# Kernel optimization log

Measured on AMD Instinct MI355X. Metric: run time of the kernel, lower is better.

The kernel has to match this reference:

```python
import jax, jax.numpy as jnp
import numpy as np

ENDING = False  # ending=False -> 'outgoing' triangle update; True -> 'incoming'
EPS = 1e-5


def _ln(x, w, b):
    m = jnp.mean(x, axis=-1, keepdims=True)
    v = jnp.mean((x - m) ** 2, axis=-1, keepdims=True)
    return (x - m) * jax.lax.rsqrt(v + EPS) * w + b


def setup_inputs() -> dict:
    key = jax.random.key(0)
    ks = jax.random.split(key, 6)
    B, N, D = 1, 384, 128
    s = 0.02
    return {
        "x": jax.random.normal(ks[0], (B, N, N, D), jnp.float32),
        "norm_in_w": jnp.ones((D,), jnp.float32),
        "norm_in_b": jnp.zeros((D,), jnp.float32),
        "w_g_in": jax.random.normal(ks[1], (2 * D, D), jnp.float32) * s,
        "w_p_in": jax.random.normal(ks[2], (2 * D, D), jnp.float32) * s,
        "w_g_out": jax.random.normal(ks[3], (D, D), jnp.float32) * s,
        "norm_out_w": jnp.ones((D,), jnp.float32),
        "norm_out_b": jnp.zeros((D,), jnp.float32),
        "w_p_out": jax.random.normal(ks[4], (D, D), jnp.float32) * s,
    }


def reference(x, norm_in_w, norm_in_b, w_g_in, w_p_in, w_g_out,
              norm_out_w, norm_out_b, w_p_out):
    D = x.shape[-1]
    xn = _ln(x, norm_in_w, norm_in_b)                       # [B,N,N,D]
    g_in = jax.nn.sigmoid(jnp.einsum('bijd,ed->bije', xn, w_g_in))  # [B,N,N,2D]
    p = jnp.einsum('bijd,ed->bije', xn, w_p_in) * g_in      # [B,N,N,2D]
    a, b = p[..., :D], p[..., D:]
    if ENDING:
        # incoming: out[i,j,d] = sum_k a[k,i,d] * b[k,j,d]
        t = jnp.einsum('bkid,bkjd->bijd', a, b)
    else:
        # outgoing: out[i,j,d] = sum_k a[i,k,d] * b[j,k,d]
        t = jnp.einsum('bikd,bjkd->bijd', a, b)
    g_out = jax.nn.sigmoid(jnp.einsum('bijd,ed->bije', xn, w_g_out))  # [B,N,N,D]
    return g_out * jnp.einsum('bijd,ed->bije', _ln(t, norm_out_w, norm_out_b), w_p_out)
```

## Files before the change

kernel.cpp:

```cpp
#include <hip/hip_runtime.h>
#include <hip/hip_bf16.h>
#include <math.h>

#define NPOS 147456
#define NSEQ 384

typedef __attribute__((ext_vector_type(4))) float f32x4;
typedef __attribute__((ext_vector_type(8))) short bf16x8;
typedef __attribute__((ext_vector_type(4))) short s16x4;

__device__ __forceinline__ unsigned short f2bf(float f){
  union { float f; unsigned u; } v; v.f = f;
  unsigned r = v.u + 0x7FFFu + ((v.u >> 16) & 1u);
  return (unsigned short)(r >> 16);
}
__device__ __forceinline__ float bf2f(unsigned short h){
  union { unsigned u; float f; } v; v.u = ((unsigned)h) << 16;
  return v.f;
}
__device__ __forceinline__ float fastsig(float x){
  return __builtin_amdgcn_rcpf(1.0f + __expf(-x));
}
__device__ __forceinline__ unsigned pk2(float lo, float hi){
  return (unsigned)f2bf(lo) | ((unsigned)f2bf(hi) << 16);
}

__global__ void wswz_all(const float* __restrict__ wgi, const float* __restrict__ wpi,
                         const float* __restrict__ wgo, const float* __restrict__ wpo,
                         unsigned short* __restrict__ wgi_s, unsigned short* __restrict__ wpi_s,
                         unsigned short* __restrict__ wgo_s, unsigned short* __restrict__ wpo_s){
  int i = blockIdx.x * 256 + threadIdx.x;
  int t = i >> 11;
  int r = i & 2047;
  const float* src; unsigned short* dst; int lt;
  if (t < 16)      { src = wgi; dst = wgi_s; lt = t;      }
  else if (t < 32) { src = wpi; dst = wpi_s; lt = t - 16; }
  else if (t < 40) { src = wgo; dst = wgo_s; lt = t - 32; }
  else             { src = wpo; dst = wpo_s; lt = t - 40; }
  int j = r & 7, lane = (r >> 3) & 63, kk = (r >> 9) & 3;
  int lrow = lane & 15, khh = lane >> 4;
  dst[lt*2048 + r] = f2bf(src[(lt*16 + lrow)*128 + kk*32 + khh*8 + j]);
}

__global__ __launch_bounds__(256, 3) void k1_ln_proj(
    const float* __restrict__ x,
    const float* __restrict__ ln_w, const float* __restrict__ ln_b,
    const unsigned short* __restrict__ wg_sw,
    const unsigned short* __restrict__ wp_sw,
    const unsigned short* __restrict__ wgo_sw,
    unsigned short* __restrict__ a_t,
    unsigned short* __restrict__ b_t,
    unsigned short* __restrict__ g_t)
{
  __shared__ unsigned short xn[128][128];
  unsigned short (*obuf)[16][136] = reinterpret_cast<unsigned short(*)[16][136]>(&xn[0][0]);

  const int tid  = threadIdx.x;
  const int posb = blockIdx.x * 128;
  const int lane = tid & 63;
  const int wid  = tid >> 6;

  const int rql = tid >> 2;
  const int q   = tid & 3;
  #pragma unroll
  for (int rr = 0; rr < 2; ++rr){
    int row = rr*64 + rql;
    const float* xr = x + (size_t)(posb + row) * 128 + q * 32;
    float v[32]; float s = 0.f, s2 = 0.f;
    #pragma unroll
    for (int j2 = 0; j2 < 8; ++j2){
      f32x4 t4 = *(const f32x4*)(xr + j2*4);
      #pragma unroll
      for (int m = 0; m < 4; ++m){ float f = t4[m]; v[j2*4+m] = f; s += f; s2 += f*f; }
    }
    s  += __shfl_xor(s, 1);  s  += __shfl_xor(s, 2);
    s2 += __shfl_xor(s2, 1); s2 += __shfl_xor(s2, 2);
    float mean = s * (1.f/128.f);
    float rstd = rsqrtf(s2 * (1.f/128.f) - mean*mean + 1e-5f);
    int sw = (row & 7) * 8;
    #pragma unroll
    for (int c = 0; c < 4; ++c){
      float n[8];
      #pragma unroll
      for (int j2 = 0; j2 < 8; ++j2){
        int k = q*32 + c*8 + j2;
        n[j2] = (v[c*8+j2] - mean) * rstd * ln_w[k] + ln_b[k];
      }
      uint4 u;
      u.x = pk2(n[0], n[1]); u.y = pk2(n[2], n[3]);
      u.z = pk2(n[4], n[5]); u.w = pk2(n[6], n[7]);
      *(uint4*)&xn[row][(q*32 + c*8) ^ sw] = u;
    }
  }
  __syncthreads();

  const int lrow = lane & 15, kh = lane >> 4;
  bf16x8 afrag[2][4];
  #pragma unroll
  for (int r = 0; r < 2; ++r){
    int row = wid*32 + r*16 + lrow;
    int sw = (row & 7) * 8;
    #pragma unroll
    for (int kk = 0; kk < 4; ++kk)
      afrag[r][kk] = *(const bf16x8*)&xn[row][(kk*32 + kh*8) ^ sw];
  }
  __syncthreads();

  const int kh4 = kh * 4;
  const int scl = wid*4 + kh;
  const int spo = lrow * 8;

#define LOADW_PAIR(G, P, et) do { \
    const unsigned short* _wg = wg_sw + (size_t)(et)*2048 + lane*8; \
    const unsigned short* _wp = wp_sw + (size_t)(et)*2048 + lane*8; \
    _Pragma("unroll") \
    for (int kk = 0; kk < 4; ++kk){ \
      G[kk] = *(const bf16x8*)(_wg + kk*512); \
      P[kk] = *(const bf16x8*)(_wp + kk*512); \
    } } while(0)

#define COMPUTE_PAIR(G, P, et) do { \
    f32x4 accg0 = {0.f,0.f,0.f,0.f}, accg1 = {0.f,0.f,0.f,0.f}; \
    f32x4 accp0 = {0.f,0.f,0.f,0.f}, accp1 = {0.f,0.f,0.f,0.f}; \
    _Pragma("unroll") \
    for (int kk = 0; kk < 4; ++kk){ \
      accg0 = __builtin_amdgcn_mfma_f32_16x16x32_bf16(afrag[0][kk], G[kk], accg0, 0, 0, 0); \
      accg1 = __builtin_amdgcn_mfma_f32_16x16x32_bf16(afrag[1][kk], G[kk], accg1, 0, 0, 0); \
      accp0 = __builtin_amdgcn_mfma_f32_16x16x32_bf16(afrag[0][kk], P[kk], accp0, 0, 0, 0); \
      accp1 = __builtin_amdgcn_mfma_f32_16x16x32_bf16(afrag[1][kk], P[kk], accp1, 0, 0, 0); \
    } \
    { uint2 u0, u1; \
      u0.x = pk2(fastsig(accg0[0])*accp0[0], fastsig(accg0[1])*accp0[1]); \
      u0.y = pk2(fastsig(accg0[2])*accp0[2], fastsig(accg0[3])*accp0[3]); \
      u1.x = pk2(fastsig(accg1[0])*accp1[0], fastsig(accg1[1])*accp1[1]); \
      u1.y = pk2(fastsig(accg1[2])*accp1[2], fastsig(accg1[3])*accp1[3]); \
      *(uint2*)&obuf[(et)&1][lrow][wid*32 + kh4]      = u0; \
      *(uint2*)&obuf[(et)&1][lrow][wid*32 + 16 + kh4] = u1; } \
    __syncthreads(); \
    { bf16x8 vv = *(const bf16x8*)&obuf[(et)&1][scl][spo]; \
      int colg = (et)*16 + scl; \
      unsigned short* dst = ((et) < 8) ? (a_t + (size_t)colg * NPOS) \
                                       : (b_t + (size_t)(colg - 128) * NPOS); \
      *(bf16x8*)(dst + posb + spo) = vv; } \
  } while(0)

  {
    bf16x8 gA[4], pA[4], gB[4], pB[4];
    LOADW_PAIR(gA, pA, 0);
    #pragma unroll
    for (int e2 = 0; e2 < 8; ++e2){
      LOADW_PAIR(gB, pB, e2*2 + 1);
      COMPUTE_PAIR(gA, pA, e2*2);
      if (e2 < 7) LOADW_PAIR(gA, pA, e2*2 + 2);
      COMPUTE_PAIR(gB, pB, e2*2 + 1);
    }
  }

#define LOADW_G(Q, et) do { \
    const unsigned short* _wq = wgo_sw + (size_t)(et)*2048 + lane*8; \
    _Pragma("unroll") \
    for (int kk = 0; kk < 4; ++kk) Q[kk] = *(const bf16x8*)(_wq + kk*512); \
  } while(0)

#define COMPUTE_G(Q, et) do { \
    f32x4 a0 = {0.f,0.f,0.f,0.f}, a1 = {0.f,0.f,0.f,0.f}; \
    _Pragma("unroll") \
    for (int kk = 0; kk < 4; ++kk){ \
      a0 = __builtin_amdgcn_mfma_f32_16x16x32_bf16(afrag[0][kk], Q[kk], a0, 0, 0, 0); \
      a1 = __builtin_amdgcn_mfma_f32_16x16x32_bf16(afrag[1][kk], Q[kk], a1, 0, 0, 0); \
    } \
    { uint2 u0, u1; \
      u0.x = pk2(fastsig(a0[0]), fastsig(a0[1])); \
      u0.y = pk2(fastsig(a0[2]), fastsig(a0[3])); \
      u1.x = pk2(fastsig(a1[0]), fastsig(a1[1])); \
      u1.y = pk2(fastsig(a1[2]), fastsig(a1[3])); \
      *(uint2*)&obuf[(et)&1][lrow][wid*32 + kh4]      = u0; \
      *(uint2*)&obuf[(et)&1][lrow][wid*32 + 16 + kh4] = u1; } \
    __syncthreads(); \
    { bf16x8 vv = *(const bf16x8*)&obuf[(et)&1][scl][spo]; \
      *(bf16x8*)(g_t + (size_t)((et)*16 + scl) * NPOS + posb + spo) = vv; } \
  } while(0)

  {
    bf16x8 qA[4], qB[4];
    LOADW_G(qA, 0);
    #pragma unroll
    for (int e2 = 0; e2 < 4; ++e2){
      LOADW_G(qB, e2*2 + 1);
      COMPUTE_G(qA, e2*2);
      if (e2 < 3) LOADW_G(qA, e2*2 + 2);
      COMPUTE_G(qB, e2*2 + 1);
    }
  }
#undef LOADW_PAIR
#undef COMPUTE_PAIR
#undef LOADW_G
#undef COMPUTE_G
}

#define K2S 72
__global__ __launch_bounds__(256) void k2_tri(
    const unsigned short* __restrict__ a_t,
    const unsigned short* __restrict__ b_t,
    unsigned short* __restrict__ t_t)
{
  __shared__ unsigned short smem[128 * K2S * 2];
  unsigned short (*As)[K2S] = (unsigned short (*)[K2S])smem;
  unsigned short (*Bs)[K2S] = (unsigned short (*)[K2S])(smem + 128 * K2S);

  const int bid  = blockIdx.x;
  const int gg   = bid >> 3;
  const int d    = (bid & 7) + 8 * (gg / 9);
  const int tile = gg % 9;
  const int i0 = (tile / 3) * 128;
  const int j0 = (tile % 3) * 128;
  const unsigned short* Ab = a_t + (size_t)d * NPOS;
  const unsigned short* Bb = b_t + (size_t)d * NPOS;

  const int tid = threadIdx.x;
  const int wid = tid >> 6, lane = tid & 63;
  const int wr = wid >> 1, wc = wid & 1;
  const int lrow = lane & 15, kh = (lane >> 4) * 8;

  f32x4 acc[4][4];
  #pragma unroll
  for (int r = 0; r < 4; ++r)
    #pragma unroll
    for (int c = 0; c < 4; ++c)
      acc[r][c] = (f32x4){0.f,0.f,0.f,0.f};

  const int sr = tid >> 1, sc = (tid & 1) * 32;

  for (int k0 = 0; k0 < NSEQ; k0 += 64){
    bf16x8 va[4], vb[4];
    #pragma unroll
    for (int j = 0; j < 4; ++j){
      va[j] = *(const bf16x8*)(Ab + (size_t)(i0 + sr) * NSEQ + k0 + sc + j*8);
      vb[j] = *(const bf16x8*)(Bb + (size_t)(j0 + sr) * NSEQ + k0 + sc + j*8);
    }
    __syncthreads();
    #pragma unroll
    for (int j = 0; j < 4; ++j){
      *(bf16x8*)&As[sr][sc + j*8] = va[j];
      *(bf16x8*)&Bs[sr][sc + j*8] = vb[j];
    }
    __syncthreads();

    #pragma unroll
    for (int kc = 0; kc < 64; kc += 32){
      bf16x8 af[4], bfr[4];
      #pragma unroll
      for (int r = 0; r < 4; ++r)
        af[r] = *(const bf16x8*)&As[wr*64 + r*16 + lrow][kc + kh];
      #pragma unroll
      for (int c = 0; c < 4; ++c)
        bfr[c] = *(const bf16x8*)&Bs[wc*64 + c*16 + lrow][kc + kh];
      #pragma unroll
      for (int r = 0; r < 4; ++r)
        #pragma unroll
        for (int c = 0; c < 4; ++c)
          acc[r][c] = __builtin_amdgcn_mfma_f32_16x16x32_bf16(af[r], bfr[c], acc[r][c], 0, 0, 0);
    }
  }

  __syncthreads();
  unsigned short (*ct)[136] = (unsigned short (*)[136])smem;
  unsigned short* Tb = t_t + (size_t)d * NPOS;
  const int lh = lane >> 4;

  #pragma unroll
  for (int p = 0; p < 2; ++p){
    if (wr == p){
      #pragma unroll
      for (int r = 0; r < 4; ++r)
        #pragma unroll
        for (int c = 0; c < 4; ++c)
          #pragma unroll
          for (int jj = 0; jj < 4; ++jj)
            ct[r*16 + lh*4 + jj][wc*64 + c*16 + lrow] = f2bf(acc[r][c][jj]);
    }
    __syncthreads();
    #pragma unroll
    for (int j = 0; j < 4; ++j){
      int row = wid*16 + j*4 + lh;
      bf16x8 v = *(const bf16x8*)&ct[row][lrow*8];
      *(bf16x8*)(Tb + (size_t)(i0 + p*64 + row) * NSEQ + j0 + lrow*8) = v;
    }
    __syncthreads();
  }
}

#define LNS 136
__global__ __launch_bounds__(256, 3) void k3_out(
    const unsigned short* __restrict__ t_t,
    const unsigned short* __restrict__ g_t,
    const float* __restrict__ ln_w, const float* __restrict__ ln_b,
    const unsigned short* __restrict__ wpo_sw,
    float* __restrict__ out)
{
  __shared__ unsigned short traw[128][136];
  __shared__ float regB[9024];
  __shared__ float smean[128], srs[128];

  const int tid = threadIdx.x;
  const int p0  = blockIdx.x * 128;
  const int lane = tid & 63, wid = tid >> 6;

  float* pps = regB;
  float* ppq = regB + 2048;
  unsigned short* lnt = (unsigned short*)regB;
  float (*ltile)[68] = (float(*)[68])regB;

  {
    int d = tid >> 1, c0 = (tid & 1) * 64;
    const unsigned short* src = t_t + (size_t)d * NPOS + p0 + c0;
    #pragma unroll
    for (int j = 0; j < 8; ++j)
      *(bf16x8*)&traw[d][c0 + j*8] = *(const bf16x8*)(src + j*8);
  }
  __syncthreads();

  const int pg = tid & 15, dh = tid >> 4;
  {
    float s8[8] = {0,0,0,0,0,0,0,0}, q8[8] = {0,0,0,0,0,0,0,0};
    #pragma unroll
    for (int jd = 0; jd < 8; ++jd){
      bf16x8 v = *(const bf16x8*)&traw[dh*8 + jd][pg*8];
      #pragma unroll
      for (int p = 0; p < 8; ++p){
        float f = bf2f((unsigned short)v[p]);
        s8[p] += f; q8[p] += f*f;
      }
    }
    #pragma unroll
    for (int p = 0; p < 8; ++p){
      pps[dh*128 + pg*8 + p] = s8[p];
      ppq[dh*128 + pg*8 + p] = q8[p];
    }
  }
  __syncthreads();
  if (tid < 128){
    float s = 0.f, q = 0.f;
    #pragma unroll
    for (int k = 0; k < 16; ++k){ s += pps[k*128 + tid]; q += ppq[k*128 + tid]; }
    float m = s * (1.f/128.f);
    smean[tid] = m;
    srs[tid]   = rsqrtf(q * (1.f/128.f) - m*m + 1e-5f);
  }
  __syncthreads();

  {
    float vv[8][8];
    #pragma unroll
    for (int jd = 0; jd < 8; ++jd){
      bf16x8 v = *(const bf16x8*)&traw[dh*8 + jd][pg*8];
      float w = ln_w[dh*8 + jd], bb = ln_b[dh*8 + jd];
      #pragma unroll
      for (int p = 0; p < 8; ++p)
        vv[jd][p] = (bf2f((unsigned short)v[p]) - smean[pg*8+p]) * srs[pg*8+p] * w + bb;
    }
    #pragma unroll
    for (int p = 0; p < 8; ++p){
      uint4 u;
      u.x = pk2(vv[0][p], vv[1][p]); u.y = pk2(vv[2][p], vv[3][p]);
      u.z = pk2(vv[4][p], vv[5][p]); u.w = pk2(vv[6][p], vv[7][p]);
      *(uint4*)&lnt[(size_t)(pg*8 + p)*LNS + dh*8] = u;
    }
  }
  __syncthreads();

  const int lrow = lane & 15, kh = (lane >> 4) * 8;
  bf16x8 af[2][4];
  #pragma unroll
  for (int r = 0; r < 2; ++r)
    #pragma unroll
    for (int kk = 0; kk < 4; ++kk)
      af[r][kk] = *(const bf16x8*)&lnt[(size_t)(wid*32 + r*16 + lrow)*LNS + kk*32 + kh];
  __syncthreads();

  {
    int e = tid >> 1, c0 = (tid & 1) * 64;
    const unsigned short* src = g_t + (size_t)e * NPOS + p0 + c0;
    #pragma unroll
    for (int j = 0; j < 8; ++j)
      *(bf16x8*)&traw[e][c0 + j*8] = *(const bf16x8*)(src + j*8);
  }
  __syncthreads();

  #pragma unroll
  for (int half = 0; half < 2; ++half){
    #pragma unroll
    for (int cf4 = 0; cf4 < 4; ++cf4){
      int cf = half*4 + cf4;
      const unsigned short* wq = wpo_sw + (size_t)cf*2048 + lane*8;
      bf16x8 bfr[4];
      #pragma unroll
      for (int kk = 0; kk < 4; ++kk)
        bfr[kk] = *(const bf16x8*)(wq + kk*512);
      f32x4 a0 = {0.f,0.f,0.f,0.f}, a1 = {0.f,0.f,0.f,0.f};
      #pragma unroll
      for (int kk = 0; kk < 4; ++kk){
        a0 = __builtin_amdgcn_mfma_f32_16x16x32_bf16(af[0][kk], bfr[kk], a0, 0, 0, 0);
        a1 = __builtin_amdgcn_mfma_f32_16x16x32_bf16(af[1][kk], bfr[kk], a1, 0, 0, 0);
      }
      int e = cf*16 + lrow;
      #pragma unroll
      for (int r = 0; r < 2; ++r){
        f32x4 av = r ? a1 : a0;
        int prow = wid*32 + r*16 + (lane >> 4)*4;
        #pragma unroll
        for (int jj = 0; jj < 4; ++jj){
          float g = bf2f(traw[e][prow + jj]);
          ltile[prow + jj][cf4*16 + lrow] = g * av[jj];
        }
      }
    }
    __syncthreads();
    {
      int pos = tid >> 1, he = tid & 1;
      const float* srcp = &ltile[pos][he*32];
      float* dst = out + (size_t)(p0 + pos)*128 + half*64 + he*32;
      #pragma unroll
      for (int j = 0; j < 8; ++j)
        *(f32x4*)(dst + j*4) = *(const f32x4*)(srcp + j*4);
    }
    __syncthreads();
  }
}

extern "C" void kernel_launch(void* const* d_in, const int* in_sizes, int n_in,
                              void* d_out, int out_size, void* d_ws, size_t ws_size,
                              hipStream_t stream) {
  (void)in_sizes; (void)n_in; (void)out_size; (void)ws_size;
  const float* x   = (const float*)d_in[0];
  const float* niw = (const float*)d_in[1];
  const float* nib = (const float*)d_in[2];
  const float* wgi = (const float*)d_in[3];
  const float* wpi = (const float*)d_in[4];
  const float* wgo = (const float*)d_in[5];
  const float* now = (const float*)d_in[6];
  const float* nob = (const float*)d_in[7];
  const float* wpo = (const float*)d_in[8];
  float* out = (float*)d_out;

  unsigned short* a_t   = (unsigned short*)d_ws;
  unsigned short* b_t   = a_t + (size_t)128 * NPOS;
  unsigned short* g_t   = b_t + (size_t)128 * NPOS;
  unsigned short* t_t   = g_t + (size_t)128 * NPOS;
  unsigned short* wgi_s = t_t + (size_t)128 * NPOS;
  unsigned short* wpi_s = wgi_s + 256 * 128;
  unsigned short* wgo_s = wpi_s + 256 * 128;
  unsigned short* wpo_s = wgo_s + 128 * 128;

  wswz_all<<<384, 256, 0, stream>>>(wgi, wpi, wgo, wpo, wgi_s, wpi_s, wgo_s, wpo_s);

  k1_ln_proj<<<NPOS/128, 256, 0, stream>>>(x, niw, nib, wgi_s, wpi_s, wgo_s, a_t, b_t, g_t);

  k2_tri<<<1152, 256, 0, stream>>>(a_t, b_t, t_t);

  k3_out<<<NPOS/128, 256, 0, stream>>>(t_t, g_t, now, nob, wpo_s, out);
}
```

Baseline: 154.0 us.

## Build LN fragments directly from swizzled smem and store output straight to global

The output kernel now XOR-swizzles the transposed t/g tiles in shared memory and builds the layer-normed MFMA A-fragments straight from the raw tile, removing the intermediate normalized-tile buffer and one barrier. The gated projection results are written directly to global memory instead of being staged through an LDS tile with a coalesced copy-out. Shared memory per block shrinks, but the global stores become scattered 4-byte writes with 128-float stride, and the element-wise LDS reads for the fragments may be slower.

```diff
diff --git a/kernel.cpp b/kernel.cpp
--- a/kernel.cpp
+++ b/kernel.cpp
@@ -290,7 +290,6 @@
   }
 }
 
-#define LNS 136
 __global__ __launch_bounds__(256, 3) void k3_out(
     const unsigned short* __restrict__ t_t,
     const unsigned short* __restrict__ g_t,
@@ -299,33 +298,31 @@
     float* __restrict__ out)
 {
   __shared__ unsigned short traw[128][136];
-  __shared__ float regB[9024];
+  __shared__ float pps[16][128];
+  __shared__ float ppq[16][128];
   __shared__ float smean[128], srs[128];
 
   const int tid = threadIdx.x;
   const int p0  = blockIdx.x * 128;
   const int lane = tid & 63, wid = tid >> 6;
 
-  float* pps = regB;
-  float* ppq = regB + 2048;
-  unsigned short* lnt = (unsigned short*)regB;
-  float (*ltile)[68] = (float(*)[68])regB;
-
   {
     int d = tid >> 1, c0 = (tid & 1) * 64;
+    int sw = ((d >> 3) & 7) * 8;
     const unsigned short* src = t_t + (size_t)d * NPOS + p0 + c0;
     #pragma unroll
     for (int j = 0; j < 8; ++j)
-      *(bf16x8*)&traw[d][c0 + j*8] = *(const bf16x8*)(src + j*8);
+      *(bf16x8*)&traw[d][(c0 + j*8) ^ sw] = *(const bf16x8*)(src + j*8);
   }
   __syncthreads();
 
   const int pg = tid & 15, dh = tid >> 4;
   {
     float s8[8] = {0,0,0,0,0,0,0,0}, q8[8] = {0,0,0,0,0,0,0,0};
+    int sw = (dh & 7) * 8;
     #pragma unroll
     for (int jd = 0; jd < 8; ++jd){
-      bf16x8 v = *(const bf16x8*)&traw[dh*8 + jd][pg*8];
+      bf16x8 v = *(const bf16x8*)&traw[dh*8 + jd][(pg*8) ^ sw];
       #pragma unroll
       for (int p = 0; p < 8; ++p){
         float f = bf2f((unsigned short)v[p]);
@@ -334,97 +331,91 @@
     }
     #pragma unroll
     for (int p = 0; p < 8; ++p){
-      pps[dh*128 + pg*8 + p] = s8[p];
-      ppq[dh*128 + pg*8 + p] = q8[p];
+      pps[dh][pg*8 + p] = s8[p];
+      ppq[dh][pg*8 + p] = q8[p];
     }
   }
   __syncthreads();
   if (tid < 128){
     float s = 0.f, q = 0.f;
     #pragma unroll
-    for (int k = 0; k < 16; ++k){ s += pps[k*128 + tid]; q += ppq[k*128 + tid]; }
+    for (int k = 0; k < 16; ++k){ s += pps[k][tid]; q += ppq[k][tid]; }
     float m = s * (1.f/128.f);
     smean[tid] = m;
     srs[tid]   = rsqrtf(q * (1.f/128.f) - m*m + 1e-5f);
   }
   __syncthreads();
 
-  {
-    float vv[8][8];
-    #pragma unroll
-    for (int jd = 0; jd < 8; ++jd){
-      bf16x8 v = *(const bf16x8*)&traw[dh*8 + jd][pg*8];
-      float w = ln_w[dh*8 + jd], bb = ln_b[dh*8 + jd];
-      #pragma unroll
-      for (int p = 0; p < 8; ++p)
-        vv[jd][p] = (bf2f((unsigned short)v[p]) - smean[pg*8+p]) * srs[pg*8+p] * w + bb;
-    }
-    #pragma unroll
-    for (int p = 0; p < 8; ++p){
-      uint4 u;
-      u.x = pk2(vv[0][p], vv[1][p]); u.y = pk2(vv[2][p], vv[3][p]);
-      u.z = pk2(vv[4][p], vv[5][p]); u.w = pk2(vv[6][p], vv[7][p]);
-      *(uint4*)&lnt[(size_t)(pg*8 + p)*LNS + dh*8] = u;
-    }
-  }
-  __syncthreads();
-
-  const int lrow = lane & 15, kh = (lane >> 4) * 8;
+  const int lrow = lane & 15, kh = lane >> 4;
+  float m2[2], rs2[2];
+  #pragma unroll
+  for (int r = 0; r < 2; ++r){
+    int pos = wid*32 + r*16 + lrow;
+    m2[r] = smean[pos];
+    rs2[r] = srs[pos];
+  }
   bf16x8 af[2][4];
   #pragma unroll
-  for (int r = 0; r < 2; ++r)
-    #pragma unroll
-    for (int kk = 0; kk < 4; ++kk)
-      af[r][kk] = *(const bf16x8*)&lnt[(size_t)(wid*32 + r*16 + lrow)*LNS + kk*32 + kh];
+  for (int kk = 0; kk < 4; ++kk){
+    int dbase = kk*32 + kh*8;
+    int sw = ((dbase >> 3) & 7) * 8;
+    f32x4 w0 = *(const f32x4*)(ln_w + dbase);
+    f32x4 w1 = *(const f32x4*)(ln_w + dbase + 4);
+    f32x4 b0 = *(const f32x4*)(ln_b + dbase);
+    f32x4 b1 = *(const f32x4*)(ln_b + dbase + 4);
+    #pragma unroll
+    for (int r = 0; r < 2; ++r){
+      int col = (wid*32 + r*16 + lrow) ^ sw;
+      float n[8];
+      #pragma unroll
+      for (int j = 0; j < 4; ++j)
+        n[j] = (bf2f(traw[dbase + j][col]) - m2[r]) * rs2[r] * w0[j] + b0[j];
+      #pragma unroll
+      for (int j = 0; j < 4; ++j)
+        n[4+j] = (bf2f(traw[dbase + 4 + j][col]) - m2[r]) * rs2[r] * w1[j] + b1[j];
+      union { uint4 u; bf16x8 v; } cvt;
+      cvt.u.x = pk2(n[0], n[1]); cvt.u.y = pk2(n[2], n[3]);
+      cvt.u.z = pk2(n[4], n[5]); cvt.u.w = pk2(n[6], n[7]);
+      af[r][kk] = cvt.v;
+    }
+  }
   __syncthreads();
 
   {
     int e = tid >> 1, c0 = (tid & 1) * 64;
+    int sw = ((e >> 3) & 7) * 8;
     const unsigned short* src = g_t + (size_t)e * NPOS + p0 + c0;
     #pragma unroll
     for (int j = 0; j < 8; ++j)
-      *(bf16x8*)&traw[e][c0 + j*8] = *(const bf16x8*)(src + j*8);
-  }
-  __syncthreads();
-
-  #pragma unroll
-  for (int half = 0; half < 2; ++half){
-    #pragma unroll
-    for (int cf4 = 0; cf4 < 4; ++cf4){
-      int cf = half*4 + cf4;
-      const unsigned short* wq = wpo_sw + (size_t)cf*2048 + lane*8;
-      bf16x8 bfr[4];
-      #pragma unroll
-      for (int kk = 0; kk < 4; ++kk)
-        bfr[kk] = *(const bf16x8*)(wq + kk*512);
-      f32x4 a0 = {0.f,0.f,0.f,0.f}, a1 = {0.f,0.f,0.f,0.f};
-      #pragma unroll
-      for (int kk = 0; kk < 4; ++kk){
-        a0 = __builtin_amdgcn_mfma_f32_16x16x32_bf16(af[0][kk], bfr[kk], a0, 0, 0, 0);
-        a1 = __builtin_amdgcn_mfma_f32_16x16x32_bf16(af[1][kk], bfr[kk], a1, 0, 0, 0);
+      *(bf16x8*)&traw[e][(c0 + j*8) ^ sw] = *(const bf16x8*)(src + j*8);
+  }
+  __syncthreads();
+
+  for (int cf = 0; cf < 8; ++cf){
+    const unsigned short* wq = wpo_sw + (size_t)cf*2048 + lane*8;
+    bf16x8 bfr[4];
+    #pragma unroll
+    for (int kk = 0; kk < 4; ++kk)
+      bfr[kk] = *(const bf16x8*)(wq + kk*512);
+    f32x4 a0 = {0.f,0.f,0.f,0.f}, a1 = {0.f,0.f,0.f,0.f};
+    #pragma unroll
+    for (int kk = 0; kk < 4; ++kk){
+      a0 = __builtin_amdgcn_mfma_f32_16x16x32_bf16(af[0][kk], bfr[kk], a0, 0, 0, 0);
+      a1 = __builtin_amdgcn_mfma_f32_16x16x32_bf16(af[1][kk], bfr[kk], a1, 0, 0, 0);
+    }
+    int e = cf*16 + lrow;
+    int esw = ((e >> 3) & 7) * 8;
+    #pragma unroll
+    for (int r = 0; r < 2; ++r){
+      f32x4 av = r ? a1 : a0;
+      int prow = wid*32 + r*16 + kh*4;
+      float* op = out + (size_t)(p0 + prow) * 128 + e;
+      #pragma unroll
+      for (int jj = 0; jj < 4; ++jj){
+        float g = bf2f(traw[e][(prow + jj) ^ esw]);
+        op[(size_t)jj * 128] = g * av[jj];
       }
-      int e = cf*16 + lrow;
-      #pragma unroll
-      for (int r = 0; r < 2; ++r){
-        f32x4 av = r ? a1 : a0;
-        int prow = wid*32 + r*16 + (lane >> 4)*4;
-        #pragma unroll
-        for (int jj = 0; jj < 4; ++jj){
-          float g = bf2f(traw[e][prow + jj]);
-          ltile[prow + jj][cf4*16 + lrow] = g * av[jj];
-        }
-      }
-    }
-    __syncthreads();
-    {
-      int pos = tid >> 1, he = tid & 1;
-      const float* srcp = &ltile[pos][he*32];
-      float* dst = out + (size_t)(p0 + pos)*128 + half*64 + he*32;
-      #pragma unroll
-      for (int j = 0; j < 8; ++j)
-        *(f32x4*)(dst + j*4) = *(const f32x4*)(srcp + j*4);
-    }
-    __syncthreads();
+    }
   }
 }
 
```

Measured after the change: 135.6 us, median of 2. -11.9%, faster.
